# Optimization experiments

Measured on AMD Instinct MI355X. Metric: run time of the kernel, lower is better.

Reference implementation:

```python
import jax, jax.numpy as jnp
import numpy as np

DIM = 96
NHEAD = 8
HEAD_DIM = DIM // NHEAD  # 12
N, L, S = 1, 262144, 262144  # 64^3 flattened 3D volume tokens
EPS_LA = 1e-6
EPS_LN = 1e-5


def layer_norm(x, w, b):
    mu = jnp.mean(x, axis=-1, keepdims=True)
    var = jnp.mean((x - mu) ** 2, axis=-1, keepdims=True)
    return (x - mu) * jax.lax.rsqrt(var + EPS_LN) * w + b


def setup_inputs() -> dict:
    key = jax.random.key(0)
    ks = jax.random.split(key, 24)
    std = 0.02
    def w(k, shape):
        return jax.random.normal(k, shape, dtype=jnp.float32) * std
    inp = {
        "mr_seg_feat_flatten": jax.random.normal(ks[0], (N, L, DIM), dtype=jnp.float32),
        "ct2mr_attention_flatten": jax.random.normal(ks[1], (N, L, DIM), dtype=jnp.float32),
        "warp_ctfeat": jax.random.normal(ks[2], (N, S, DIM), dtype=jnp.float32),
        # CrossmodalSemanticsCalibration params (torch Linear weights: [out, in])
        "w_qkv": w(ks[3], (DIM, DIM)),
        "w_qkv2": w(ks[4], (DIM, DIM)),
        "ln1_w": jnp.ones((DIM,), jnp.float32),
        "ln1_b": jnp.zeros((DIM,), jnp.float32),
        "ln2_w": jnp.ones((2 * DIM,), jnp.float32),
        "ln2_b": jnp.zeros((2 * DIM,), jnp.float32),
        "mlp_fc1_w": w(ks[5], (2 * DIM, 2 * DIM)),
        "mlp_fc1_b": jnp.zeros((2 * DIM,), jnp.float32),
        "mlp_fc2_w": w(ks[6], (DIM, 2 * DIM)),
        "mlp_fc2_b": jnp.zeros((DIM,), jnp.float32),
        # StructureAttention(96, 8) params
        "sa_wq": w(ks[7], (DIM, DIM)),
        "sa_wk": w(ks[8], (DIM, DIM)),
        "sa_wv": w(ks[9], (DIM, DIM)),
        "sa_merge": w(ks[10], (DIM, DIM)),
        "sa_mlp_w1": w(ks[11], (2 * DIM, 2 * DIM)),
        "sa_mlp_w2": w(ks[12], (DIM, 2 * DIM)),
        "sa_ln1_w": jnp.ones((DIM,), jnp.float32),
        "sa_ln1_b": jnp.zeros((DIM,), jnp.float32),
        "sa_ln2_w": jnp.ones((DIM,), jnp.float32),
        "sa_ln2_b": jnp.zeros((DIM,), jnp.float32),
    }
    return inp


def _forward(mr_seg_feat_flatten, ct2mr_attention_flatten, warp_ctfeat,
             w_qkv, w_qkv2, ln1_w, ln1_b, ln2_w, ln2_b,
             mlp_fc1_w, mlp_fc1_b, mlp_fc2_w, mlp_fc2_b,
             sa_wq, sa_wk, sa_wv, sa_merge, sa_mlp_w1, sa_mlp_w2,
             sa_ln1_w, sa_ln1_b, sa_ln2_w, sa_ln2_b):
    # CrossmodalSemanticsCalibration.forward (ct2mr_attention_flatten is unused, as in torch)
    x0 = layer_norm(mr_seg_feat_flatten, ln1_w, ln1_b)
    shortcut = x0 @ w_qkv.T                        # [N, L, C]
    y = shortcut @ w_qkv2.T                        # [N, L, C]

    # StructureAttention(y, warp_ctfeat) with kernelized LinearAttention
    n, l, c = y.shape
    s = warp_ctfeat.shape[1]
    q = (y @ sa_wq.T).reshape(n, l, NHEAD, HEAD_DIM)
    k = (warp_ctfeat @ sa_wk.T).reshape(n, s, NHEAD, HEAD_DIM)
    v = (warp_ctfeat @ sa_wv.T).reshape(n, s, NHEAD, HEAD_DIM)
    Q = jax.nn.elu(q) + 1.0
    K = jax.nn.elu(k) + 1.0
    KV = jnp.einsum('nshd,nshv->nhdv', K, v / s)   # [N, H, d, d]
    Z = 1.0 / (jnp.einsum('nlhd,nhd->nlh', Q, K.sum(axis=1)) + EPS_LA)
    msg = jnp.einsum('nlhd,nhdv,nlh->nlhv', Q, KV, Z) * s
    msg = msg.reshape(n, l, c) @ sa_merge.T
    msg = layer_norm(msg, sa_ln1_w, sa_ln1_b)
    h = jnp.concatenate([y, msg], axis=-1) @ sa_mlp_w1.T
    h = jax.nn.relu(h) @ sa_mlp_w2.T
    h = layer_norm(h, sa_ln2_w, sa_ln2_b)
    x = y + h                                      # StructureAttention output

    # fuse with shortcut, final Mlp (GELU, exact erf as torch default)
    x = jnp.concatenate([x, shortcut], axis=-1)    # [N, L, 2C]
    x = layer_norm(x, ln2_w, ln2_b)
    x = jax.nn.gelu(x @ mlp_fc1_w.T + mlp_fc1_b, approximate=False)
    x = x @ mlp_fc2_w.T + mlp_fc2_b
    return x                                       # [N, L, C]


def reference(mr_seg_feat_flatten, ct2mr_attention_flatten, warp_ctfeat,
              w_qkv, w_qkv2, ln1_w, ln1_b, ln2_w, ln2_b,
              mlp_fc1_w, mlp_fc1_b, mlp_fc2_w, mlp_fc2_b,
              sa_wq, sa_wk, sa_wv, sa_merge, sa_mlp_w1, sa_mlp_w2,
              sa_ln1_w, sa_ln1_b, sa_ln2_w, sa_ln2_b):
    return _forward(mr_seg_feat_flatten, ct2mr_attention_flatten, warp_ctfeat,
                    w_qkv, w_qkv2, ln1_w, ln1_b, ln2_w, ln2_b,
                    mlp_fc1_w, mlp_fc1_b, mlp_fc2_w, mlp_fc2_b,
                    sa_wq, sa_wk, sa_wv, sa_merge, sa_mlp_w1, sa_mlp_w2,
                    sa_ln1_w, sa_ln1_b, sa_ln2_w, sa_ln2_b)
```

## Files before the change

### kernel.cpp

```cpp
#include <hip/hip_runtime.h>
#include <hip/hip_bf16.h>


typedef __attribute__((ext_vector_type(8))) short short8;
typedef __attribute__((ext_vector_type(4))) float f32x4;
typedef __attribute__((ext_vector_type(4))) unsigned int uint4v;

#define WS_FLAG 0
#define WS_PKV  512
#define WS_PSV  (WS_PKV + 16*9216*4)
#define WS_PSE  (WS_PSV + 16*96*4)
#define WS_KSUM (WS_PSE + 16*96*4)
#define WS_KSTOT (WS_KSUM + 96*4)
#define WS_CM   (WS_KSTOT + 64)
#define WS_BDT  (WS_CM + 768*4)
#define WS_WB   (WS_BDT + 9216*2)
#define WS_VEC  (WS_WB + 165888*2)

#define OQKV   0
#define OQKV2  9216
#define OWQ    18432
#define OWK    27648
#define OWV    36864
#define OMERGE 46080
#define OW1    55296
#define OW2    92160
#define OFC1   110592
#define OFC2   147456
#define VLN1W 0
#define VLN1B 96
#define VLN2W 192
#define VLN2B 384
#define VFC1B 576
#define VFC2B 768
#define VSA1W 864
#define VSA1B 960
#define VSA2W 1056
#define VSA2B 1152

struct InPtrs { const void* p[23]; };

__device__ inline float b2f(unsigned short x) {
  union { unsigned u; float f; } c; c.u = ((unsigned)x) << 16; return c.f;
}
__device__ inline unsigned short f2b(float f) {
  __hip_bfloat16 h = __float2bfloat16(f);
  return *(unsigned short*)&h;
}
__device__ inline uint2 pack4bf(float v0, float v1, float v2, float v3) {
  uint2 r;
  r.x = (unsigned)f2b(v0) | ((unsigned)f2b(v1) << 16);
  r.y = (unsigned)f2b(v2) | ((unsigned)f2b(v3) << 16);
  return r;
}

__global__ void probe_k(const void* in0, unsigned* flag) {
  int tid = threadIdx.x;
  const unsigned short* u = (const unsigned short*)in0;
  int cnt = 0;
  for (int j = 0; j < 8; ++j) {
    unsigned short v = u[(tid * 8 + j) * 2];
    unsigned e = (v >> 7) & 0xFF;
    if ((e >= 110 && e <= 141) || ((v & 0x7FFF) == 0)) cnt++;
  }
  for (int o = 32; o; o >>= 1) cnt += __shfl_down(cnt, o);
  if (tid == 0) *flag = (cnt > 256) ? 1u : 0u;
}

template<int ISBF>
__launch_bounds__(256)
__global__ void prep_k(InPtrs ip, char* ws) {
  if (((const unsigned*)ws)[0] != (unsigned)ISBF) return;
  const int wsrc[10] = {3,4,13,14,15,16,17,18,9,11};
  const int wdst[11] = {0,9216,18432,27648,36864,46080,55296,92160,110592,147456,165888};
  const int vsrc[10] = {5,6,7,8,10,12,19,20,21,22};
  const int vdst[11] = {0,96,192,384,576,768,864,960,1056,1152,1248};
  unsigned short* wb = (unsigned short*)(ws + WS_WB);
  float* vec = (float*)(ws + WS_VEC);
  float* zr = (float*)(ws + WS_PKV);
  const int TOT = 165888 + 1248 + 150528;
  for (int e = blockIdx.x * 256 + threadIdx.x; e < TOT; e += gridDim.x * 256) {
    if (e < 165888) {
      int w = 0;
      while (w < 9 && e >= wdst[w + 1]) ++w;
      int loc = e - wdst[w];
      if (ISBF) wb[e] = ((const unsigned short*)ip.p[wsrc[w]])[loc];
      else      wb[e] = f2b(((const float*)ip.p[wsrc[w]])[loc]);
    } else if (e < 165888 + 1248) {
      int e2 = e - 165888;
      int w = 0;
      while (w < 9 && e2 >= vdst[w + 1]) ++w;
      int loc = e2 - vdst[w];
      vec[e2] = ISBF ? b2f(((const unsigned short*)ip.p[vsrc[w]])[loc])
                     : ((const float*)ip.p[vsrc[w]])[loc];
    } else {
      zr[e - 165888 - 1248] = 0.0f;
    }
  }
}

template<int NB, int NCF, int KSTEPS>
__device__ inline void domm(const unsigned short* A, int apitch,
                            const unsigned short* B, int bpitch, int cf0,
                            int lane, f32x4 (&acc)[NB][NCF]) {
  int lr = lane & 15, lg = lane >> 4;
#pragma unroll
  for (int ks = 0; ks < KSTEPS; ++ks) {
    int k0 = ks * 32 + lg * 8;
    short8 bf[NCF];
#pragma unroll
    for (int cf = 0; cf < NCF; ++cf)
      bf[cf] = *(const short8*)(B + ((cf0 + cf) * 16 + lr) * bpitch + k0);
    short8 af[NB];
#pragma unroll
    for (int b = 0; b < NB; ++b)
      af[b] = *(const short8*)(A + (b * 16 + lr) * apitch + k0);
#pragma unroll
    for (int cf = 0; cf < NCF; ++cf)
#pragma unroll
      for (int b = 0; b < NB; ++b)
        acc[b][cf] = __builtin_amdgcn_mfma_f32_16x16x32_bf16(af[b], bf[cf], acc[b][cf], 0, 0, 0);
  }
}

template<int NB, int NCF>
__device__ inline void writeFrags(unsigned short* dst, int pitch, int cf0,
                                  int lane, f32x4 (&acc)[NB][NCF]) {
  int lr = lane & 15, lg = lane >> 4;
#pragma unroll
  for (int b = 0; b < NB; ++b)
#pragma unroll
    for (int cf = 0; cf < NCF; ++cf)
#pragma unroll
      for (int r = 0; r < 4; ++r) {
        float v = acc[b][cf][r];
        float v1 = __shfl_xor(v, 1);
        float v2 = __shfl_xor(v, 2);
        float v3 = __shfl_xor(v, 3);
        if ((lane & 3) == 0) {
          int row = b * 16 + lg * 4 + r;
          int col = (cf0 + cf) * 16 + lr;
          *(uint2*)(dst + row * pitch + col) = pack4bf(v, v1, v2, v3);
        }
      }
}

template<int NB, int NCF>
__device__ inline void zacc(f32x4 (&acc)[NB][NCF]) {
#pragma unroll
  for (int b = 0; b < NB; ++b)
#pragma unroll
    for (int cf = 0; cf < NCF; ++cf)
      acc[b][cf] = (f32x4){0.f, 0.f, 0.f, 0.f};
}

template<int ISBF>
__launch_bounds__(256)
__global__ void kA(const void* ct_, char* ws) {
  if (((const unsigned*)ws)[0] != (unsigned)ISBF) return;
  __shared__ unsigned short sCT[64][104];
  __shared__ unsigned short sEK[96][72];
  __shared__ unsigned short sVT[96][72];
  const unsigned short* Wb = (const unsigned short*)(ws + WS_WB);
  float* pKV = (float*)(ws + WS_PKV);
  int tid = threadIdx.x, lane = tid & 63, wid = tid >> 6;
  int lr = lane & 15, lg = lane >> 4;

  f32x4 kvacc[2][6];
  zacc<2, 6>(kvacc);
  float accEk = 0.f, accV = 0.f;

  for (int t = blockIdx.x; t < 4096; t += gridDim.x) {
    if (ISBF) {
      const uint4v* src = (const uint4v*)((const unsigned short*)ct_ + (size_t)t * 6144);
#pragma unroll
      for (int i = 0; i < 3; ++i) {
        int ch = tid * 3 + i;
        int r = ch / 12, c = (ch % 12) * 8;
        *(uint4v*)&sCT[r][c] = src[ch];
      }
    } else {
      const float4* src = (const float4*)((const float*)ct_ + (size_t)t * 6144);
#pragma unroll
      for (int i = 0; i < 6; ++i) {
        int ch = tid * 6 + i;
        int r = ch / 24, c = (ch % 24) * 4;
        float4 v = src[ch];
        *(uint2*)&sCT[r][c] = pack4bf(v.x, v.y, v.z, v.w);
      }
    }
    __syncthreads();

    const unsigned short* Wp = Wb + ((wid < 2) ? OWK : OWV);
    int cf0 = (wid & 1) * 3;
    f32x4 pacc[4][3];
    zacc<4, 3>(pacc);
    domm<4, 3, 3>(&sCT[0][0], 104, Wp, 96, cf0, lane, pacc);
    if (wid < 2) {
#pragma unroll
      for (int b = 0; b < 4; ++b)
#pragma unroll
        for (int cf = 0; cf < 3; ++cf)
#pragma unroll
          for (int r = 0; r < 4; ++r) {
            float v = pacc[b][cf][r];
            pacc[b][cf][r] = v > 0.f ? v : expm1f(v);
          }
    }
    {
      unsigned short* dstT = (wid < 2) ? &sEK[0][0] : &sVT[0][0];
#pragma unroll
      for (int b = 0; b < 4; ++b)
#pragma unroll
        for (int cf = 0; cf < 3; ++cf) {
          int col = (cf0 + cf) * 16 + lr;
          int t0 = b * 16 + lg * 4;
          *(uint2*)(dstT + col * 72 + t0) =
              pack4bf(pacc[b][cf][0], pacc[b][cf][1], pacc[b][cf][2], pacc[b][cf][3]);
        }
    }
    __syncthreads();

    if (wid < 3) {
#pragma unroll
      for (int ks = 0; ks < 2; ++ks) {
        int k0 = ks * 32 + lg * 8;
        short8 a[2];
#pragma unroll
        for (int bb = 0; bb < 2; ++bb)
          a[bb] = *(const short8*)&sEK[(wid * 2 + bb) * 16 + lr][k0];
#pragma unroll
        for (int cf = 0; cf < 6; ++cf) {
          short8 vb = *(const short8*)&sVT[cf * 16 + lr][k0];
#pragma unroll
          for (int bb = 0; bb < 2; ++bb)
            kvacc[bb][cf] = __builtin_amdgcn_mfma_f32_16x16x32_bf16(a[bb], vb, kvacc[bb][cf], 0, 0, 0);
        }
      }
    }
    if (tid < 96) {
#pragma unroll
      for (int j = 0; j < 8; ++j) {
        short8 e = *(const short8*)&sEK[tid][j * 8];
        short8 v = *(const short8*)&sVT[tid][j * 8];
#pragma unroll
        for (int qq = 0; qq < 8; ++qq) {
          accEk += b2f((unsigned short)e[qq]);
          accV  += b2f((unsigned short)v[qq]);
        }
      }
    }
    __syncthreads();
  }

  int slice = blockIdx.x & 15;
  if (tid < 96) {
    atomicAdd((float*)(ws + WS_PSE) + slice * 96 + tid, accEk);
    atomicAdd((float*)(ws + WS_PSV) + slice * 96 + tid, accV);
  }
  if (wid < 3) {
#pragma unroll
    for (int bb = 0; bb < 2; ++bb)
#pragma unroll
      for (int cf = 0; cf < 6; ++cf)
#pragma unroll
        for (int r = 0; r < 4; ++r) {
          int hd = (wid * 2 + bb) * 16 + lg * 4 + r;
          int hv = cf * 16 + lr;
          if (hd / 12 == hv / 12)
            atomicAdd(&pKV[slice * 9216 + hd * 96 + hv], kvacc[bb][cf][r]);
        }
  }
}

template<int ISBF>
__launch_bounds__(256)
__global__ void kFin(const void* merge_, char* ws) {
  if (((const unsigned*)ws)[0] != (unsigned)ISBF) return;
  __shared__ float Ks[96], sV[96], KV[8][12][12], csk[96];
  int tid = threadIdx.x;
  const float* pSE = (const float*)(ws + WS_PSE);
  const float* pSV = (const float*)(ws + WS_PSV);
  const float* pKV = (const float*)(ws + WS_PKV);
  if (tid < 96) {
    float a = 0.f, b = 0.f;
    for (int s = 0; s < 16; ++s) { a += pSE[s * 96 + tid]; b += pSV[s * 96 + tid]; }
    Ks[tid] = 262144.0f + a;
    sV[tid] = b;
    ((float*)(ws + WS_KSUM))[tid] = Ks[tid];
  }
  __syncthreads();
  if (tid < 8) {
    float s = 0.f;
    for (int d = 0; d < 12; ++d) s += Ks[tid * 12 + d];
    ((float*)(ws + WS_KSTOT))[tid] = s;
  }
  for (int e = tid; e < 1152; e += 256) {
    int h = e / 144, r = e % 144, d = r / 12, v = r % 12;
    int hd = h * 12 + d, hv = h * 12 + v;
    float s = sV[hv];
    for (int sl = 0; sl < 16; ++sl) s += pKV[sl * 9216 + hd * 96 + hv];
    KV[h][d][v] = s * (1.0f / 262144.0f);
  }
  unsigned short* bdt = (unsigned short*)(ws + WS_BDT);
  for (int e = tid; e < 9216; e += 256) bdt[e] = 0;
  __syncthreads();
  for (int e = tid; e < 1152; e += 256) {
    int h = e / 144, r = e % 144, d = r / 12, v = r % 12;
    bdt[(h * 12 + v) * 96 + (h * 12 + d)] = f2b(KV[h][d][v]);
  }
  if (tid < 96) {
    int h = tid / 12, v = tid % 12;
    float s = 0.f;
    for (int d = 0; d < 12; ++d) s += KV[h][d][v];
    csk[tid] = s;
  }
  __syncthreads();
  for (int e = tid; e < 768; e += 256) {
    int h = e / 96, c = e % 96;
    float s = 0.f;
    for (int v = 0; v < 12; ++v) {
      float mg = ISBF ? b2f(((const unsigned short*)merge_)[c * 96 + h * 12 + v])
                      : ((const float*)merge_)[c * 96 + h * 12 + v];
      s += csk[h * 12 + v] * mg;
    }
    ((float*)(ws + WS_CM))[e] = s;
  }
}

template<int ISBF>
__launch_bounds__(256, 2)
__global__ void kB(const void* mr_, void* out_, char* ws) {
  if (((const unsigned*)ws)[0] != (unsigned)ISBF) return;
  __shared__ unsigned short sA[64][200];
  __shared__ unsigned short sS[64][104];
  __shared__ unsigned short sY[64][96];
  __shared__ float sZs[64][8];
  const unsigned short* Wb = (const unsigned short*)(ws + WS_WB);
  const float* vec  = (const float*)(ws + WS_VEC);
  const float* Ksum = (const float*)(ws + WS_KSUM);
  const float* KsTot = (const float*)(ws + WS_KSTOT);
  const float* CM = (const float*)(ws + WS_CM);
  const unsigned short* BDT = (const unsigned short*)(ws + WS_BDT);
  int tid = threadIdx.x, lane = tid & 63, wid = tid >> 6;
  int lr = lane & 15, lg = lane >> 4;
  int w16 = wid * 16;
  int row = tid >> 1, c0 = (tid & 1) * 48;
  int tok0 = blockIdx.x * 64;

  if (ISBF) {
    const uint4v* src = (const uint4v*)((const unsigned short*)mr_ + (size_t)tok0 * 96);
#pragma unroll
    for (int i = 0; i < 3; ++i) {
      int ch = tid * 3 + i;
      int r = ch / 12, c = (ch % 12) * 8;
      *(uint4v*)&sA[r][c] = src[ch];
    }
  } else {
    const float4* src = (const float4*)((const float*)mr_ + (size_t)tok0 * 96);
#pragma unroll
    for (int i = 0; i < 6; ++i) {
      int ch = tid * 6 + i;
      int r = ch / 24, c = (ch % 24) * 4;
      float4 v = src[ch];
      *(uint2*)&sA[r][c] = pack4bf(v.x, v.y, v.z, v.w);
    }
  }
  __syncthreads();

  if (tid < 128) {
    float vals[48];
    float s = 0.f;
#pragma unroll
    for (int i = 0; i < 6; ++i) {
      short8 v = *(const short8*)&sA[row][c0 + i * 8];
#pragma unroll
      for (int j = 0; j < 8; ++j) {
        float x = b2f((unsigned short)v[j]);
        vals[i * 8 + j] = x; s += x;
      }
    }
    s += __shfl_xor(s, 1);
    float mean = s * (1.f / 96.f);
    float s2 = 0.f;
#pragma unroll
    for (int j = 0; j < 48; ++j) { float d = vals[j] - mean; s2 += d * d; }
    s2 += __shfl_xor(s2, 1);
    float rs = rsqrtf(s2 * (1.f / 96.f) + 1e-5f);
#pragma unroll
    for (int i = 0; i < 6; ++i) {
      short8 o;
#pragma unroll
      for (int j = 0; j < 8; ++j) {
        int c = c0 + i * 8 + j;
        o[j] = (short)f2b((vals[i * 8 + j] - mean) * rs * vec[VLN1W + c] + vec[VLN1B + c]);
      }
      *(short8*)&sA[row][c0 + i * 8] = o;
    }
  }
  __syncthreads();

  f32x4 a6[1][6];
  f32x4 a12[1][12];

  zacc<1, 6>(a6);
  domm<1, 6, 3>(&sA[w16][0], 200, Wb + OQKV, 96, 0, lane, a6);
  writeFrags<1, 6>(&sS[w16][0], 104, 0, lane, a6);
  __syncthreads();

  zacc<1, 6>(a6);
  domm<1, 6, 3>(&sS[w16][0], 104, Wb + OQKV2, 96, 0, lane, a6);
  writeFrags<1, 6>(&sY[w16][0], 96, 0, lane, a6);
  __syncthreads();

  zacc<1, 6>(a6);
  domm<1, 6, 3>(&sY[w16][0], 96, Wb + OWQ, 96, 0, lane, a6);
#pragma unroll
  for (int cf = 0; cf < 6; ++cf)
#pragma unroll
    for (int r = 0; r < 4; ++r) {
      float v = a6[0][cf][r];
      a6[0][cf][r] = v > 0.f ? v : expm1f(v);
    }
  writeFrags<1, 6>(&sA[w16][0], 200, 0, lane, a6);
  __syncthreads();

#pragma unroll
  for (int i = 0; i < 2; ++i) {
    int task = tid + 256 * i;
    int zr = task >> 3, h = task & 7;
    float den = KsTot[h];
#pragma unroll
    for (int d = 0; d < 12; ++d)
      den += b2f(sA[zr][h * 12 + d]) * Ksum[h * 12 + d];
    sZs[zr][h] = 262144.0f / (den + 1e-6f);
  }
  __syncthreads();

  zacc<1, 6>(a6);
  domm<1, 6, 3>(&sA[w16][0], 200, BDT, 96, 0, lane, a6);
#pragma unroll
  for (int cf = 0; cf < 6; ++cf) {
    int col = cf * 16 + lr;
    int h = col / 12;
#pragma unroll
    for (int r = 0; r < 4; ++r) {
      int rw = w16 + lg * 4 + r;
      a6[0][cf][r] *= sZs[rw][h];
    }
  }
  writeFrags<1, 6>(&sA[w16][96], 200, 0, lane, a6);
  __syncthreads();

  zacc<1, 6>(a6);
  domm<1, 6, 3>(&sA[w16][96], 200, Wb + OMERGE, 96, 0, lane, a6);
  writeFrags<1, 6>(&sA[w16][0], 200, 0, lane, a6);
  __syncthreads();

  if (tid < 128) {
    float vals[48];
#pragma unroll
    for (int j = 0; j < 48; ++j) vals[j] = 0.f;
#pragma unroll
    for (int h = 0; h < 8; ++h) {
      float zh = sZs[row][h];
      const float* cmr = CM + h * 96 + c0;
#pragma unroll
      for (int j = 0; j < 48; j += 4) {
        float4 c4 = *(const float4*)(cmr + j);
        vals[j] += zh * c4.x; vals[j + 1] += zh * c4.y;
        vals[j + 2] += zh * c4.z; vals[j + 3] += zh * c4.w;
      }
    }
    float s = 0.f;
#pragma unroll
    for (int i = 0; i < 6; ++i) {
      short8 v = *(const short8*)&sA[row][c0 + i * 8];
#pragma unroll
      for (int j = 0; j < 8; ++j) {
        float x = vals[i * 8 + j] + b2f((unsigned short)v[j]);
        vals[i * 8 + j] = x; s += x;
      }
    }
    s += __shfl_xor(s, 1);
    float mean = s * (1.f / 96.f);
    float s2 = 0.f;
#pragma unroll
    for (int j = 0; j < 48; ++j) { float d = vals[j] - mean; s2 += d * d; }
    s2 += __shfl_xor(s2, 1);
    float rs = rsqrtf(s2 * (1.f / 96.f) + 1e-5f);
#pragma unroll
    for (int i = 0; i < 6; ++i) {
      short8 o;
#pragma unroll
      for (int j = 0; j < 8; ++j) {
        int c = c0 + i * 8 + j;
        o[j] = (short)f2b((vals[i * 8 + j] - mean) * rs * vec[VSA1W + c] + vec[VSA1B + c]);
      }
      *(short8*)&sA[row][96 + c0 + i * 8] = o;
    }
#pragma unroll
    for (int i = 0; i < 6; ++i)
      *(uint4v*)&sA[row][c0 + i * 8] = *(const uint4v*)&sY[row][c0 + i * 8];
  }
  __syncthreads();

  zacc<1, 12>(a12);
  domm<1, 12, 6>(&sA[w16][0], 200, Wb + OW1, 192, 0, lane, a12);
#pragma unroll
  for (int cf = 0; cf < 12; ++cf)
#pragma unroll
    for (int r = 0; r < 4; ++r)
      a12[0][cf][r] = fmaxf(a12[0][cf][r], 0.f);
  __syncthreads();
  writeFrags<1, 12>(&sA[w16][0], 200, 0, lane, a12);
  __syncthreads();

  zacc<1, 6>(a6);
  domm<1, 6, 6>(&sA[w16][0], 200, Wb + OW2, 192, 0, lane, a6);
  __syncthreads();
  writeFrags<1, 6>(&sA[w16][0], 200, 0, lane, a6);
  __syncthreads();

  if (tid < 128) {
    float vals[48], sv[48];
    float s = 0.f;
#pragma unroll
    for (int i = 0; i < 6; ++i) {
      short8 v = *(const short8*)&sA[row][c0 + i * 8];
#pragma unroll
      for (int j = 0; j < 8; ++j) {
        float x = b2f((unsigned short)v[j]);
        vals[i * 8 + j] = x; s += x;
      }
    }
    s += __shfl_xor(s, 1);
    float mh = s * (1.f / 96.f);
    float s2 = 0.f;
#pragma unroll
    for (int j = 0; j < 48; ++j) { float d = vals[j] - mh; s2 += d * d; }
    s2 += __shfl_xor(s2, 1);
    float rh = rsqrtf(s2 * (1.f / 96.f) + 1e-5f);
    float sx = 0.f;
#pragma unroll
    for (int j = 0; j < 48; ++j) {
      int c = c0 + j;
      float x = b2f(sY[row][c]) + (vals[j] - mh) * rh * vec[VSA2W + c] + vec[VSA2B + c];
      vals[j] = x; sx += x;
    }
#pragma unroll
    for (int j = 0; j < 48; ++j) {
      float v = b2f(sS[row][c0 + j]);
      sv[j] = v; sx += v;
    }
    sx += __shfl_xor(sx, 1);
    float m2 = sx * (1.f / 192.f);
    float sx2 = 0.f;
#pragma unroll
    for (int j = 0; j < 48; ++j) { float d = vals[j] - m2; sx2 += d * d; }
#pragma unroll
    for (int j = 0; j < 48; ++j) { float d = sv[j] - m2; sx2 += d * d; }
    sx2 += __shfl_xor(sx2, 1);
    float r2 = rsqrtf(sx2 * (1.f / 192.f) + 1e-5f);
#pragma unroll
    for (int i = 0; i < 6; ++i) {
      short8 oa, ob;
#pragma unroll
      for (int j = 0; j < 8; ++j) {
        int idx = i * 8 + j, c = c0 + idx;
        oa[j] = (short)f2b((vals[idx] - m2) * r2 * vec[VLN2W + c] + vec[VLN2B + c]);
        ob[j] = (short)f2b((sv[idx] - m2) * r2 * vec[VLN2W + 96 + c] + vec[VLN2B + 96 + c]);
      }
      *(short8*)&sA[row][c0 + i * 8] = oa;
      *(short8*)&sA[row][96 + c0 + i * 8] = ob;
    }
  }
  __syncthreads();

  zacc<1, 12>(a12);
  domm<1, 12, 6>(&sA[w16][0], 200, Wb + OFC1, 192, 0, lane, a12);
#pragma unroll
  for (int cf = 0; cf < 12; ++cf) {
    float bb = vec[VFC1B + cf * 16 + lr];
#pragma unroll
    for (int r = 0; r < 4; ++r) {
      float x = a12[0][cf][r] + bb;
      a12[0][cf][r] = 0.5f * x * (1.0f + erff(x * 0.70710678118f));
    }
  }
  __syncthreads();
  writeFrags<1, 12>(&sA[w16][0], 200, 0, lane, a12);
  __syncthreads();

  zacc<1, 6>(a6);
  domm<1, 6, 6>(&sA[w16][0], 200, Wb + OFC2, 192, 0, lane, a6);
#pragma unroll
  for (int cf = 0; cf < 6; ++cf) {
    int col = cf * 16 + lr;
    float bias = vec[VFC2B + col];
#pragma unroll
    for (int r = 0; r < 4; ++r) {
      float v = a6[0][cf][r] + bias;
      float v1 = __shfl_xor(v, 1);
      float v2 = __shfl_xor(v, 2);
      float v3 = __shfl_xor(v, 3);
      if ((lane & 3) == 0) {
        size_t token = (size_t)tok0 + w16 + lg * 4 + r;
        size_t off = token * 96 + col;
        if (ISBF) {
          *(uint2*)((unsigned short*)out_ + off) = pack4bf(v, v1, v2, v3);
        } else {
          float4 f; f.x = v; f.y = v1; f.z = v2; f.w = v3;
          *(float4*)((float*)out_ + off) = f;
        }
      }
    }
  }
}

extern "C" void kernel_launch(void* const* d_in, const int* in_sizes, int n_in,
                              void* d_out, int out_size, void* d_ws, size_t ws_size,
                              hipStream_t stream) {
  (void)in_sizes; (void)n_in; (void)out_size; (void)ws_size;
  char* ws = (char*)d_ws;
  probe_k<<<1, 64, 0, stream>>>(d_in[0], (unsigned*)ws);
  InPtrs ip;
  for (int i = 0; i < 23; ++i) ip.p[i] = d_in[i];
  prep_k<0><<<512, 256, 0, stream>>>(ip, ws);
  prep_k<1><<<512, 256, 0, stream>>>(ip, ws);
  kA<0><<<1024, 256, 0, stream>>>(d_in[2], ws);
  kA<1><<<1024, 256, 0, stream>>>(d_in[2], ws);
  kFin<0><<<1, 256, 0, stream>>>(d_in[16], ws);
  kFin<1><<<1, 256, 0, stream>>>(d_in[16], ws);
  kB<0><<<4096, 256, 0, stream>>>(d_in[0], d_out, ws);
  kB<1><<<4096, 256, 0, stream>>>(d_in[0], d_out, ws);
}
```

Baseline: 835.0 us.

## Drop sS shared buffer, stash shortcut in registers, use all threads for row ops

Removes the separate sS shared-memory tile by writing the qkv output into the upper half of sA and keeping each thread's slice of the shortcut in registers (sstash) until the final LayerNorm. Row-wise LayerNorm phases now use all 256 threads, four per row with 24 columns each, instead of 128 threads with 48 columns. The first MLP matmul reads sY and sA directly in two K-halves instead of copying sY into sA. Launch bounds are raised to 3 blocks per SM to exploit the smaller LDS footprint, which tightens the register budget and risks spills.

```diff
diff --git a/kernel.cpp b/kernel.cpp
--- a/kernel.cpp
+++ b/kernel.cpp
@@ -329,11 +329,10 @@
 }
 
 template<int ISBF>
-__launch_bounds__(256, 2)
+__launch_bounds__(256, 3)
 __global__ void kB(const void* mr_, void* out_, char* ws) {
   if (((const unsigned*)ws)[0] != (unsigned)ISBF) return;
   __shared__ unsigned short sA[64][200];
-  __shared__ unsigned short sS[64][104];
   __shared__ unsigned short sY[64][96];
   __shared__ float sZs[64][8];
   const unsigned short* Wb = (const unsigned short*)(ws + WS_WB);
@@ -345,8 +344,10 @@
   int tid = threadIdx.x, lane = tid & 63, wid = tid >> 6;
   int lr = lane & 15, lg = lane >> 4;
   int w16 = wid * 16;
-  int row = tid >> 1, c0 = (tid & 1) * 48;
+  int row = tid >> 2, c0 = (tid & 3) * 24;
   int tok0 = blockIdx.x * 64;
+
+  short8 sstash[3];
 
   if (ISBF) {
     const uint4v* src = (const uint4v*)((const unsigned short*)mr_ + (size_t)tok0 * 96);
@@ -368,11 +369,11 @@
   }
   __syncthreads();
 
-  if (tid < 128) {
-    float vals[48];
+  {
+    float vals[24];
     float s = 0.f;
 #pragma unroll
-    for (int i = 0; i < 6; ++i) {
+    for (int i = 0; i < 3; ++i) {
       short8 v = *(const short8*)&sA[row][c0 + i * 8];
 #pragma unroll
       for (int j = 0; j < 8; ++j) {
@@ -380,15 +381,15 @@
         vals[i * 8 + j] = x; s += x;
       }
     }
-    s += __shfl_xor(s, 1);
+    s += __shfl_xor(s, 1); s += __shfl_xor(s, 2);
     float mean = s * (1.f / 96.f);
     float s2 = 0.f;
 #pragma unroll
-    for (int j = 0; j < 48; ++j) { float d = vals[j] - mean; s2 += d * d; }
-    s2 += __shfl_xor(s2, 1);
+    for (int j = 0; j < 24; ++j) { float d = vals[j] - mean; s2 += d * d; }
+    s2 += __shfl_xor(s2, 1); s2 += __shfl_xor(s2, 2);
     float rs = rsqrtf(s2 * (1.f / 96.f) + 1e-5f);
 #pragma unroll
-    for (int i = 0; i < 6; ++i) {
+    for (int i = 0; i < 3; ++i) {
       short8 o;
 #pragma unroll
       for (int j = 0; j < 8; ++j) {
@@ -405,11 +406,14 @@
 
   zacc<1, 6>(a6);
   domm<1, 6, 3>(&sA[w16][0], 200, Wb + OQKV, 96, 0, lane, a6);
-  writeFrags<1, 6>(&sS[w16][0], 104, 0, lane, a6);
-  __syncthreads();
-
+  writeFrags<1, 6>(&sA[w16][96], 200, 0, lane, a6);
+  __syncthreads();
+
+#pragma unroll
+  for (int i = 0; i < 3; ++i)
+    sstash[i] = *(const short8*)&sA[row][96 + c0 + i * 8];
   zacc<1, 6>(a6);
-  domm<1, 6, 3>(&sS[w16][0], 104, Wb + OQKV2, 96, 0, lane, a6);
+  domm<1, 6, 3>(&sA[w16][96], 200, Wb + OQKV2, 96, 0, lane, a6);
   writeFrags<1, 6>(&sY[w16][0], 96, 0, lane, a6);
   __syncthreads();
 
@@ -457,16 +461,16 @@
   writeFrags<1, 6>(&sA[w16][0], 200, 0, lane, a6);
   __syncthreads();
 
-  if (tid < 128) {
-    float vals[48];
-#pragma unroll
-    for (int j = 0; j < 48; ++j) vals[j] = 0.f;
+  {
+    float vals[24];
+#pragma unroll
+    for (int j = 0; j < 24; ++j) vals[j] = 0.f;
 #pragma unroll
     for (int h = 0; h < 8; ++h) {
       float zh = sZs[row][h];
       const float* cmr = CM + h * 96 + c0;
 #pragma unroll
-      for (int j = 0; j < 48; j += 4) {
+      for (int j = 0; j < 24; j += 4) {
         float4 c4 = *(const float4*)(cmr + j);
         vals[j] += zh * c4.x; vals[j + 1] += zh * c4.y;
         vals[j + 2] += zh * c4.z; vals[j + 3] += zh * c4.w;
@@ -474,7 +478,7 @@
     }
     float s = 0.f;
 #pragma unroll
-    for (int i = 0; i < 6; ++i) {
+    for (int i = 0; i < 3; ++i) {
       short8 v = *(const short8*)&sA[row][c0 + i * 8];
 #pragma unroll
       for (int j = 0; j < 8; ++j) {
@@ -482,15 +486,15 @@
         vals[i * 8 + j] = x; s += x;
       }
     }
-    s += __shfl_xor(s, 1);
+    s += __shfl_xor(s, 1); s += __shfl_xor(s, 2);
     float mean = s * (1.f / 96.f);
     float s2 = 0.f;
 #pragma unroll
-    for (int j = 0; j < 48; ++j) { float d = vals[j] - mean; s2 += d * d; }
-    s2 += __shfl_xor(s2, 1);
+    for (int j = 0; j < 24; ++j) { float d = vals[j] - mean; s2 += d * d; }
+    s2 += __shfl_xor(s2, 1); s2 += __shfl_xor(s2, 2);
     float rs = rsqrtf(s2 * (1.f / 96.f) + 1e-5f);
 #pragma unroll
-    for (int i = 0; i < 6; ++i) {
+    for (int i = 0; i < 3; ++i) {
       short8 o;
 #pragma unroll
       for (int j = 0; j < 8; ++j) {
@@ -499,14 +503,12 @@
       }
       *(short8*)&sA[row][96 + c0 + i * 8] = o;
     }
-#pragma unroll
-    for (int i = 0; i < 6; ++i)
-      *(uint4v*)&sA[row][c0 + i * 8] = *(const uint4v*)&sY[row][c0 + i * 8];
   }
   __syncthreads();
 
   zacc<1, 12>(a12);
-  domm<1, 12, 6>(&sA[w16][0], 200, Wb + OW1, 192, 0, lane, a12);
+  domm<1, 12, 3>(&sY[w16][0], 96, Wb + OW1, 192, 0, lane, a12);
+  domm<1, 12, 3>(&sA[w16][96], 200, Wb + OW1 + 96, 192, 0, lane, a12);
 #pragma unroll
   for (int cf = 0; cf < 12; ++cf)
 #pragma unroll
@@ -522,11 +524,11 @@
   writeFrags<1, 6>(&sA[w16][0], 200, 0, lane, a6);
   __syncthreads();
 
-  if (tid < 128) {
-    float vals[48], sv[48];
+  {
+    float vals[24];
     float s = 0.f;
 #pragma unroll
-    for (int i = 0; i < 6; ++i) {
+    for (int i = 0; i < 3; ++i) {
       short8 v = *(const short8*)&sA[row][c0 + i * 8];
 #pragma unroll
       for (int j = 0; j < 8; ++j) {
@@ -534,42 +536,47 @@
         vals[i * 8 + j] = x; s += x;
       }
     }
-    s += __shfl_xor(s, 1);
+    s += __shfl_xor(s, 1); s += __shfl_xor(s, 2);
     float mh = s * (1.f / 96.f);
     float s2 = 0.f;
 #pragma unroll
-    for (int j = 0; j < 48; ++j) { float d = vals[j] - mh; s2 += d * d; }
-    s2 += __shfl_xor(s2, 1);
+    for (int j = 0; j < 24; ++j) { float d = vals[j] - mh; s2 += d * d; }
+    s2 += __shfl_xor(s2, 1); s2 += __shfl_xor(s2, 2);
     float rh = rsqrtf(s2 * (1.f / 96.f) + 1e-5f);
     float sx = 0.f;
 #pragma unroll
-    for (int j = 0; j < 48; ++j) {
+    for (int j = 0; j < 24; ++j) {
       int c = c0 + j;
       float x = b2f(sY[row][c]) + (vals[j] - mh) * rh * vec[VSA2W + c] + vec[VSA2B + c];
       vals[j] = x; sx += x;
     }
 #pragma unroll
-    for (int j = 0; j < 48; ++j) {
-      float v = b2f(sS[row][c0 + j]);
-      sv[j] = v; sx += v;
-    }
-    sx += __shfl_xor(sx, 1);
+    for (int i = 0; i < 3; ++i)
+#pragma unroll
+      for (int j = 0; j < 8; ++j)
+        sx += b2f((unsigned short)sstash[i][j]);
+    sx += __shfl_xor(sx, 1); sx += __shfl_xor(sx, 2);
     float m2 = sx * (1.f / 192.f);
     float sx2 = 0.f;
 #pragma unroll
-    for (int j = 0; j < 48; ++j) { float d = vals[j] - m2; sx2 += d * d; }
-#pragma unroll
-    for (int j = 0; j < 48; ++j) { float d = sv[j] - m2; sx2 += d * d; }
-    sx2 += __shfl_xor(sx2, 1);
+    for (int j = 0; j < 24; ++j) { float d = vals[j] - m2; sx2 += d * d; }
+#pragma unroll
+    for (int i = 0; i < 3; ++i)
+#pragma unroll
+      for (int j = 0; j < 8; ++j) {
+        float d = b2f((unsigned short)sstash[i][j]) - m2; sx2 += d * d;
+      }
+    sx2 += __shfl_xor(sx2, 1); sx2 += __shfl_xor(sx2, 2);
     float r2 = rsqrtf(sx2 * (1.f / 192.f) + 1e-5f);
 #pragma unroll
-    for (int i = 0; i < 6; ++i) {
+    for (int i = 0; i < 3; ++i) {
       short8 oa, ob;
 #pragma unroll
       for (int j = 0; j < 8; ++j) {
         int idx = i * 8 + j, c = c0 + idx;
         oa[j] = (short)f2b((vals[idx] - m2) * r2 * vec[VLN2W + c] + vec[VLN2B + c]);
-        ob[j] = (short)f2b((sv[idx] - m2) * r2 * vec[VLN2W + 96 + c] + vec[VLN2B + 96 + c]);
+        float sv = b2f((unsigned short)sstash[i][j]);
+        ob[j] = (short)f2b((sv - m2) * r2 * vec[VLN2W + 96 + c] + vec[VLN2B + 96 + c]);
       }
       *(short8*)&sA[row][c0 + i * 8] = oa;
       *(short8*)&sA[row][96 + c0 + i * 8] = ob;
```

Measured after the change: 766.2 us. 8.2% less time.
